# Optimization experiments

Measured on AMD Instinct MI355X. Metric: run time of the kernel, lower is better.

Reference implementation:

```python
import jax, jax.numpy as jnp
from jax import lax
import numpy as np

STEP = 0.01
BS = 32  # blocksize


def conv(x, w, b=None, stride=1, pad=0):
    y = lax.conv_general_dilated(x, w, (stride, stride), [(pad, pad), (pad, pad)],
                                 dimension_numbers=('NCHW', 'OIHW', 'NCHW'))
    if b is not None:
        y = y + b[None, :, None, None]
    return y


def prelu(x, a):
    return jnp.where(x >= 0, x, a * x)


def depth_to_space(x, bs):
    # matches Reshape_Concat_Adap: each [C] pixel vector viewed as (C', bs, bs)
    B, C, h, w = x.shape
    C2 = C // (bs * bs)
    y = x.reshape(B, C2, bs, bs, h, w)
    y = y.transpose(0, 1, 4, 2, 5, 3)  # B, C2, h, bs, w, bs
    return y.reshape(B, C2, h * bs, w * bs)


def setup_inputs() -> dict:
    key = jax.random.key(0)
    ks = jax.random.split(key, 32)

    def W(k, shape):
        fan_in = shape[1] * shape[2] * shape[3]
        return (jax.random.normal(k, shape, jnp.float32) * np.sqrt(2.0 / fan_in)).astype(jnp.float32)

    inp = {
        'x': jax.random.normal(ks[0], (4, 1, 192, 192), jnp.float32),
        'epoch': 1,
        'd1_w': W(ks[1], (16, 1, 4, 4)),
        'd2_w': W(ks[2], (256, 16, 4, 4)),
        'd3_w': W(ks[3], (1024, 256, 2, 2)),
        'd4_w': W(ks[4], (154, 1024, 1, 1)),
        'q1_w': W(ks[5], (154, 154, 1, 1)), 'q1_b': jnp.zeros((154,), jnp.float32),
        'q2_w': W(ks[6], (154, 154, 1, 1)), 'q2_b': jnp.zeros((154,), jnp.float32),
        'q3_w': W(ks[7], (154, 154, 1, 1)), 'q3_b': jnp.zeros((154,), jnp.float32),
        'up_w': W(ks[8], (1024, 154, 1, 1)), 'up_b': jnp.zeros((1024,), jnp.float32),
        'c1_w': W(ks[9], (64, 1, 3, 3)), 'c1_b': jnp.zeros((64,), jnp.float32), 'c1_a': jnp.float32(0.25),
        'c2_w': W(ks[10], (64, 64, 3, 3)), 'c2_b': jnp.zeros((64,), jnp.float32), 'c2_a': jnp.float32(0.25),
        'c3_w': W(ks[11], (64, 64, 3, 3)), 'c3_b': jnp.zeros((64,), jnp.float32), 'c3_a': jnp.float32(0.25),
        'c4_w': W(ks[12], (64, 64, 3, 3)), 'c4_b': jnp.zeros((64,), jnp.float32), 'c4_a': jnp.float32(0.25),
        'c5_w': W(ks[13], (256, 64, 3, 3)), 'c5_b': jnp.zeros((256,), jnp.float32),
    }
    return inp


def reference(x, epoch, d1_w, d2_w, d3_w, d4_w, q1_w, q1_b, q2_w, q2_b, q3_w, q3_b,
              up_w, up_b, c1_w, c1_b, c1_a, c2_w, c2_b, c2_a, c3_w, c3_b, c3_a,
              c4_w, c4_b, c4_a, c5_w, c5_b):
    step = jnp.float32(STEP)
    relu = jax.nn.relu
    # down path
    h = relu(conv(x, d1_w, stride=4))
    h = relu(conv(h, d2_w, stride=4))
    h = relu(conv(h, d3_w, stride=2))
    x4 = conv(h, d4_w)                      # [B,154,H/32,W/32]
    # STE quantize + dequantize
    q = x4 + lax.stop_gradient(jnp.floor(x4 / step) - x4)
    xr = q * step
    t = xr
    t = relu(conv(t, q1_w, q1_b)) + t
    t = relu(conv(t, q2_w, q2_b)) + t
    t = relu(conv(t, q3_w, q3_b)) + t
    x_comp = t + xr
    # upsample to blocksize^2 channels, then depth-to-space
    u = conv(x_comp, up_w, up_b)            # [B,1024,H/32,W/32]
    y = depth_to_space(u, BS)               # [B,1,H,W]
    # refinement CNN
    b1 = prelu(conv(y, c1_w, c1_b, pad=1), c1_a)
    b2 = prelu(conv(b1 + y, c2_w, c2_b, pad=1), c2_a)
    b3 = prelu(conv(b2 + b1, c3_w, c3_b, pad=1), c3_a)
    b4 = prelu(conv(b3 + b2, c4_w, c4_b, pad=1), c4_a)
    b5 = conv(b4 + b3, c5_w, c5_b, pad=1)   # [B,256,H,W]
    B, _, H, Wd = b5.shape
    return (b5.reshape(B, 1, 256, H, Wd), x_comp, x4)
```

## Files before the change

### kernel.cpp

```cpp
#include <hip/hip_runtime.h>
#include <math.h>

#define N_B 4
#define IMG 192
#define P 194

typedef __attribute__((ext_vector_type(8))) short short8;
typedef __attribute__((ext_vector_type(4))) float f32x4;

__device__ __forceinline__ unsigned f2bf(float f) {
  unsigned u = __float_as_uint(f);
  return (u + 0x7fffu + ((u >> 16) & 1u)) >> 16;
}
__device__ __forceinline__ float bf2f(unsigned b) {
  return __uint_as_float(b << 16);
}
__device__ __forceinline__ int swz(int pix) {
  return (pix & 7) << 4;
}
__device__ __forceinline__ void gload_lds16(const void* g, void* l) {
  __builtin_amdgcn_global_load_lds(
      (const __attribute__((address_space(1))) void*)g,
      (__attribute__((address_space(3))) void*)l, 16, 0, 0);
}

__global__ void k_d1(const float* __restrict__ x, const float* __restrict__ w,
                     float* __restrict__ out) {
  int idx = blockIdx.x * 256 + threadIdx.x;
  if (idx >= N_B * 16 * 48 * 48) return;
  int xq = idx % 48; int t = idx / 48; int yq = t % 48; t /= 48;
  int oc = t % 16; int b = t / 16;
  const float* xp = x + (b * IMG + yq * 4) * IMG + xq * 4;
  const float* wp = w + oc * 16;
  float s = 0.f;
#pragma unroll
  for (int dy = 0; dy < 4; ++dy)
#pragma unroll
    for (int dx = 0; dx < 4; ++dx)
      s = fmaf(xp[dy * IMG + dx], wp[dy * 4 + dx], s);
  out[idx] = fmaxf(s, 0.f);
}

__global__ void k_d2(const float* __restrict__ h1, const float* __restrict__ w,
                     float* __restrict__ out) {
  int idx = blockIdx.x * 256 + threadIdx.x;
  if (idx >= N_B * 256 * 12 * 12) return;
  int xq = idx % 12; int t = idx / 12; int yq = t % 12; t /= 12;
  int oc = t % 256; int b = t / 256;
  float s = 0.f;
  for (int ci = 0; ci < 16; ++ci) {
    const float* ip = h1 + ((b * 16 + ci) * 48 + yq * 4) * 48 + xq * 4;
    const float* wp = w + (oc * 16 + ci) * 16;
#pragma unroll
    for (int dy = 0; dy < 4; ++dy)
#pragma unroll
      for (int dx = 0; dx < 4; ++dx)
        s = fmaf(ip[dy * 48 + dx], wp[dy * 4 + dx], s);
  }
  out[((size_t)b * 144 + yq * 12 + xq) * 256 + oc] = fmaxf(s, 0.f);
}

__global__ __launch_bounds__(256) void k_wd3(const float* __restrict__ w,
                                             float* __restrict__ o) {
  int idx = blockIdx.x * 256 + threadIdx.x;
  if (idx >= 4 * 256 * 1024) return;
  int oc = idx & 1023; int ci = (idx >> 10) & 255; int tap = idx >> 18;
  o[idx] = w[((size_t)oc * 256 + ci) * 4 + tap];
}

__global__ __launch_bounds__(256) void k_d3(const float* __restrict__ h2t,
                                            const float* __restrict__ w3p,
                                            float* __restrict__ out) {
  int idx = blockIdx.x * 256 + threadIdx.x;
  if (idx >= N_B * 36 * 1024) return;
  int oc = idx & 1023; int t = idx >> 10; int p6 = t % 36; int b = t / 36;
  int yq = p6 / 6, xq = p6 % 6;
  const float* p00 = h2t + ((size_t)b * 144 + (2 * yq) * 12 + 2 * xq) * 256;
  const float* p01 = p00 + 256;
  const float* p10 = p00 + 12 * 256;
  const float* p11 = p10 + 256;
  const float* w0 = w3p + oc;
  float a0 = 0.f, a1 = 0.f, a2 = 0.f, a3 = 0.f;
  for (int ci = 0; ci < 256; ++ci) {
    a0 = fmaf(p00[ci], w0[(size_t)(0 * 256 + ci) * 1024], a0);
    a1 = fmaf(p01[ci], w0[(size_t)(1 * 256 + ci) * 1024], a1);
    a2 = fmaf(p10[ci], w0[(size_t)(2 * 256 + ci) * 1024], a2);
    a3 = fmaf(p11[ci], w0[(size_t)(3 * 256 + ci) * 1024], a3);
  }
  out[((size_t)b * 36 + p6) * 1024 + oc] = fmaxf((a0 + a1) + (a2 + a3), 0.f);
}

__global__ __launch_bounds__(512) void k_mid(
    const float* __restrict__ h3t, const float* __restrict__ d4_w,
    const float* __restrict__ q1_w, const float* __restrict__ q1_b,
    const float* __restrict__ q2_w, const float* __restrict__ q2_b,
    const float* __restrict__ q3_w, const float* __restrict__ q3_b,
    const float* __restrict__ up_w, const float* __restrict__ up_b,
    float* __restrict__ x4_out, float* __restrict__ xcomp_out,
    float* __restrict__ y_out) {
  __shared__ float hv[1024];
  __shared__ float part[512];
  __shared__ float tv[160];
  __shared__ float xrv[160];
  int blk = blockIdx.x;
  int b = blk / 36, p = blk % 36;
  int tid = threadIdx.x;
  for (int i = tid; i < 1024; i += 512) hv[i] = h3t[(size_t)blk * 1024 + i];
  __syncthreads();
  {
    int half = tid >> 8, oc = tid & 255;
    float s = 0.f;
    if (oc < 154) {
      const float* wp = d4_w + (size_t)oc * 1024 + half * 512;
      const float* hp = hv + half * 512;
      float a0 = 0.f, a1 = 0.f, a2 = 0.f, a3 = 0.f;
      for (int i = 0; i < 512; i += 4) {
        a0 = fmaf(hp[i], wp[i], a0);
        a1 = fmaf(hp[i + 1], wp[i + 1], a1);
        a2 = fmaf(hp[i + 2], wp[i + 2], a2);
        a3 = fmaf(hp[i + 3], wp[i + 3], a3);
      }
      s = (a0 + a1) + (a2 + a3);
    }
    part[tid] = s;
  }
  __syncthreads();
  if (tid < 154) {
    float s = part[tid] + part[tid + 256];
    x4_out[(b * 154 + tid) * 36 + p] = s;
    float q = floorf(s / 0.01f) * 0.01f;
    xrv[tid] = q;
    tv[tid] = q;
  }
  __syncthreads();
  const float* qw[3] = {q1_w, q2_w, q3_w};
  const float* qb[3] = {q1_b, q2_b, q3_b};
  for (int l = 0; l < 3; ++l) {
    float s = 0.f;
    if (tid < 154) {
      const float* wp = qw[l] + (size_t)tid * 154;
      float a0 = 0.f, a1 = 0.f;
      int i = 0;
      for (; i + 1 < 154; i += 2) {
        a0 = fmaf(tv[i], wp[i], a0);
        a1 = fmaf(tv[i + 1], wp[i + 1], a1);
      }
      if (i < 154) a0 = fmaf(tv[i], wp[i], a0);
      s = qb[l][tid] + a0 + a1;
    }
    __syncthreads();
    if (tid < 154) tv[tid] = fmaxf(s, 0.f) + tv[tid];
    __syncthreads();
  }
  if (tid < 154) {
    float xc = tv[tid] + xrv[tid];
    tv[tid] = xc;
    xcomp_out[(b * 154 + tid) * 36 + p] = xc;
  }
  __syncthreads();
  int h = p / 6, w6 = p % 6;
#pragma unroll
  for (int k = 0; k < 2; ++k) {
    int co = k * 512 + tid;
    const float* wp = up_w + (size_t)co * 154;
    float a0 = 0.f, a1 = 0.f;
    int i = 0;
    for (; i + 1 < 154; i += 2) {
      a0 = fmaf(tv[i], wp[i], a0);
      a1 = fmaf(tv[i + 1], wp[i + 1], a1);
    }
    if (i < 154) a0 = fmaf(tv[i], wp[i], a0);
    float s = up_b[co] + a0 + a1;
    int i32 = co >> 5, j = co & 31;
    y_out[(b * IMG + h * 32 + i32) * IMG + w6 * 32 + j] = s;
  }
}

__global__ __launch_bounds__(256) void k_ring(short* s0, short* s1,
                                              short* s2, short* s3) {
  int idx = blockIdx.x * 256 + threadIdx.x;
  if (idx >= 4 * 4 * 772 * 8) return;
  int chunk = idx & 7; int t = idx >> 3;
  int r = t % 772; t /= 772; int b = t % 4; int buf = t / 4;
  int y, x;
  if (r < 194) { y = 0; x = r; }
  else if (r < 388) { y = 193; x = r - 194; }
  else { int q = r - 388; y = 1 + (q >> 1); x = (q & 1) ? 193 : 0; }
  short* p = (buf == 0) ? s0 : (buf == 1) ? s1 : (buf == 2) ? s2 : s3;
  *(uint4*)(p + (((size_t)b * P + y) * P + x) * 64 + chunk * 8) =
      make_uint4(0u, 0u, 0u, 0u);
}

__global__ __launch_bounds__(256) void k_c1b(const float* __restrict__ y,
                                             const float* __restrict__ w,
                                             const float* __restrict__ bias,
                                             const float* __restrict__ a_p,
                                             short* __restrict__ B1,
                                             short* __restrict__ S1) {
  int idx = blockIdx.x * 256 + threadIdx.x;
  if (idx >= N_B * IMG * IMG) return;
  int X = idx % IMG; int t = idx / IMG; int Y = t % IMG; int b = t / IMG;
  float p[9];
#pragma unroll
  for (int dy = 0; dy < 3; ++dy)
#pragma unroll
    for (int dx = 0; dx < 3; ++dx) {
      int gy = Y + dy - 1, gx = X + dx - 1;
      p[dy * 3 + dx] = ((unsigned)gy < (unsigned)IMG && (unsigned)gx < (unsigned)IMG)
                           ? y[(b * IMG + gy) * IMG + gx]
                           : 0.f;
    }
  float a = *a_p;
  float yc = p[4];
  size_t base = (((size_t)b * P + Y + 1) * P + X + 1) * 64;
  for (int oc = 0; oc < 64; oc += 8) {
    unsigned bw[4], sw[4];
#pragma unroll
    for (int j = 0; j < 8; ++j) {
      float s = bias[oc + j];
      const float* wq = w + (oc + j) * 9;
#pragma unroll
      for (int k = 0; k < 9; ++k) s = fmaf(p[k], wq[k], s);
      s = s >= 0.f ? s : a * s;
      float sv = s + yc;
      if (j & 1) { bw[j >> 1] |= f2bf(s) << 16; sw[j >> 1] |= f2bf(sv) << 16; }
      else       { bw[j >> 1] = f2bf(s);        sw[j >> 1] = f2bf(sv); }
    }
    *(uint4*)(B1 + base + oc) = make_uint4(bw[0], bw[1], bw[2], bw[3]);
    *(uint4*)(S1 + base + oc) = make_uint4(sw[0], sw[1], sw[2], sw[3]);
  }
}

__global__ __launch_bounds__(256) void k_wprep4(
    const float* __restrict__ w2, const float* __restrict__ w3,
    const float* __restrict__ w4, const float* __restrict__ w5,
    short* __restrict__ o2, short* __restrict__ o3,
    short* __restrict__ o4, short* __restrict__ o5) {
  int which = blockIdx.y;
  const float* w = (which == 0) ? w2 : (which == 1) ? w3 : (which == 2) ? w4 : w5;
  short* o = (which == 0) ? o2 : (which == 1) ? o3 : (which == 2) ? o4 : o5;
  int OC = (which == 3) ? 256 : 64;
  int idx = blockIdx.x * 256 + threadIdx.x;
  if (idx >= OC * 64 * 9) return;
  int ic = idx & 63; int t = idx >> 6; int r = t % OC; int tap = t / OC;
  int oc = (which < 3) ? (((r >> 2) & 3) * 16 + ((r >> 4) & 3) * 4 + (r & 3)) : r;
  int ks = ic >> 5, lg = (ic >> 3) & 3, j = ic & 7, li = r & 15, ocblk = r >> 4;
  size_t dst = ((size_t)(tap * 2 + ks) * (OC >> 4) + ocblk) * 512 +
               (lg * 16 + li) * 8 + j;
  o[dst] = (short)f2bf(w[((size_t)oc * 64 + ic) * 9 + tap]);
}

template <int MODE>
__global__ __launch_bounds__(256) void k_conv3x3n(
    const short* __restrict__ sin, const short* __restrict__ bprev,
    const short* __restrict__ wbf, const float* __restrict__ bias,
    const float* __restrict__ a_p, short* __restrict__ bout,
    short* __restrict__ sout) {
  __shared__ __align__(16) char smem[300 * 128];
  int tid = threadIdx.x;
  int b = blockIdx.z;
  int x0 = blockIdx.x * 48, y0 = blockIdx.y * 4;
  int w = tid >> 6, lane = tid & 63, li = lane & 15, lg = lane >> 4;

  for (int c = w; c < 38; c += 4) {
    int o = c * 1024 + lane * 16;
    if (o < 300 * 128) {
      int pix = o >> 7;
      int icq = ((o >> 4) & 7) ^ (pix & 7);
      const short* src = sin +
          (((size_t)b * P + y0 + pix / 50) * P + x0 + pix % 50) * 64 + icq * 8;
      gload_lds16(src, smem + c * 1024);
    }
  }
  __syncthreads();

  const short* abase = wbf + (lane << 3);
  const int astride = 64 * 32;

  f32x4 acc[4][3];
#pragma unroll
  for (int mt = 0; mt < 4; ++mt)
#pragma unroll
    for (int nt = 0; nt < 3; ++nt) acc[mt][nt] = (f32x4){0.f, 0.f, 0.f, 0.f};

#define LOADA(s, dst)                                                          \
  {                                                                            \
    const short* p_ = abase + (size_t)(s) * astride;                           \
    _Pragma("unroll") for (int mt = 0; mt < 4; ++mt)                           \
        dst[mt] = *(const short8*)(p_ + mt * 512);                             \
  }
#define LOADB(s, dst)                                                          \
  {                                                                            \
    const int tap_ = (s) >> 1, ks_ = (s) & 1;                                  \
    const int dy_ = tap_ / 3, dx_ = tap_ % 3;                                  \
    _Pragma("unroll") for (int nt = 0; nt < 3; ++nt) {                         \
      int pix_ = (w + dy_) * 50 + nt * 16 + dx_ + li;                          \
      int byte_ = (pix_ * 128 + ks_ * 64 + lg * 16) ^ swz(pix_);               \
      dst[nt] = *(const short8*)(smem + byte_);                                \
    }                                                                          \
  }

  short8 Abuf[2][4];
  short8 Bbuf[3];
  LOADA(0, Abuf[0]);
#pragma unroll
  for (int s = 0; s < 18; ++s) {
    if (s + 1 < 18) LOADA(s + 1, Abuf[(s + 1) & 1]);
    LOADB(s, Bbuf);
    short8* Ac = Abuf[s & 1];
#pragma unroll
    for (int mt = 0; mt < 4; ++mt)
#pragma unroll
      for (int nt = 0; nt < 3; ++nt)
        acc[mt][nt] = __builtin_amdgcn_mfma_f32_16x16x32_bf16(Ac[mt], Bbuf[nt],
                                                              acc[mt][nt], 0, 0, 0);
  }
#undef LOADA
#undef LOADB

  float a = *a_p;
  int gy = y0 + w;
#pragma unroll
  for (int nt = 0; nt < 3; ++nt) {
    int gx = x0 + nt * 16 + li;
    float r[16];
#pragma unroll
    for (int mt = 0; mt < 4; ++mt) {
      float4 bv = *(const float4*)(bias + lg * 16 + mt * 4);
      f32x4 v = acc[mt][nt];
      float t0 = v[0] + bv.x, t1 = v[1] + bv.y, t2 = v[2] + bv.z, t3 = v[3] + bv.w;
      r[mt * 4 + 0] = t0 >= 0.f ? t0 : a * t0;
      r[mt * 4 + 1] = t1 >= 0.f ? t1 : a * t1;
      r[mt * 4 + 2] = t2 >= 0.f ? t2 : a * t2;
      r[mt * 4 + 3] = t3 >= 0.f ? t3 : a * t3;
    }
    size_t pi = (((size_t)b * P + gy + 1) * P + gx + 1) * 64 + lg * 16;
    if (MODE == 0) {
      uint4 u0 = make_uint4(f2bf(r[0]) | (f2bf(r[1]) << 16),
                            f2bf(r[2]) | (f2bf(r[3]) << 16),
                            f2bf(r[4]) | (f2bf(r[5]) << 16),
                            f2bf(r[6]) | (f2bf(r[7]) << 16));
      uint4 u1 = make_uint4(f2bf(r[8]) | (f2bf(r[9]) << 16),
                            f2bf(r[10]) | (f2bf(r[11]) << 16),
                            f2bf(r[12]) | (f2bf(r[13]) << 16),
                            f2bf(r[14]) | (f2bf(r[15]) << 16));
      *(uint4*)(bout + pi) = u0;
      *(uint4*)(bout + pi + 8) = u1;
    }
    uint4 p0 = *(const uint4*)(bprev + pi);
    uint4 p1 = *(const uint4*)(bprev + pi + 8);
    unsigned pw[8] = {p0.x, p0.y, p0.z, p0.w, p1.x, p1.y, p1.z, p1.w};
    unsigned so[8];
#pragma unroll
    for (int k = 0; k < 8; ++k) {
      float s0 = r[2 * k] + bf2f(pw[k] & 0xffffu);
      float s1 = r[2 * k + 1] + bf2f(pw[k] >> 16);
      so[k] = f2bf(s0) | (f2bf(s1) << 16);
    }
    *(uint4*)(sout + pi) = make_uint4(so[0], so[1], so[2], so[3]);
    *(uint4*)(sout + pi + 8) = make_uint4(so[4], so[5], so[6], so[7]);
  }
}

__global__ __launch_bounds__(256) void k_conv3x3b5(
    const short* __restrict__ sin, const short* __restrict__ wbf,
    const float* __restrict__ bias, float* __restrict__ fout) {
  __shared__ __align__(16) char smem[340 * 128];
  int tid = threadIdx.x;
  int g = blockIdx.z & 3, b = blockIdx.z >> 2;
  int x0 = blockIdx.x * 32, y0 = blockIdx.y * 8;
  int w = tid >> 6, lane = tid & 63, li = lane & 15, lg = lane >> 4;

  for (int c = w; c < 43; c += 4) {
    int o = c * 1024 + lane * 16;
    if (o < 340 * 128) {
      int pix = o >> 7;
      int icq = ((o >> 4) & 7) ^ (pix & 7);
      const short* src = sin +
          (((size_t)b * P + y0 + pix / 34) * P + x0 + pix % 34) * 64 + icq * 8;
      gload_lds16(src, smem + c * 1024);
    }
  }
  __syncthreads();

  int row0 = 2 * w;
  const short* abase = wbf + (size_t)(g << 2) * 512 + (lane << 3);
  const int astride = 256 * 32;

  f32x4 acc[4][4];
#pragma unroll
  for (int mt = 0; mt < 4; ++mt)
#pragma unroll
    for (int nt = 0; nt < 4; ++nt) acc[mt][nt] = (f32x4){0.f, 0.f, 0.f, 0.f};

#define LOADA5(s, dst)                                                         \
  {                                                                            \
    const short* p_ = abase + (size_t)(s) * astride;                           \
    _Pragma("unroll") for (int mt = 0; mt < 4; ++mt)                           \
        dst[mt] = *(const short8*)(p_ + mt * 512);                             \
  }
#define LOADB5(s, dst)                                                         \
  {                                                                            \
    const int tap_ = (s) >> 1, ks_ = (s) & 1;                                  \
    const int dy_ = tap_ / 3, dx_ = tap_ % 3;                                  \
    _Pragma("unroll") for (int nt = 0; nt < 4; ++nt) {                         \
      int pix_ = (row0 + (nt >> 1) + dy_) * 34 + (nt & 1) * 16 + dx_ + li;     \
      int byte_ = (pix_ * 128 + ks_ * 64 + lg * 16) ^ swz(pix_);               \
      dst[nt] = *(const short8*)(smem + byte_);                                \
    }                                                                          \
  }

  short8 Abuf[2][4];
  short8 Bbuf[4];
  LOADA5(0, Abuf[0]);
#pragma unroll
  for (int s = 0; s < 18; ++s) {
    if (s + 1 < 18) LOADA5(s + 1, Abuf[(s + 1) & 1]);
    LOADB5(s, Bbuf);
    short8* Ac = Abuf[s & 1];
#pragma unroll
    for (int mt = 0; mt < 4; ++mt)
#pragma unroll
      for (int nt = 0; nt < 4; ++nt)
        acc[mt][nt] = __builtin_amdgcn_mfma_f32_16x16x32_bf16(Bbuf[nt], Ac[mt],
                                                              acc[mt][nt], 0, 0, 0);
  }
#undef LOADA5
#undef LOADB5

#pragma unroll
  for (int nt = 0; nt < 4; ++nt) {
    int gy = y0 + row0 + (nt >> 1);
    int gx = x0 + (nt & 1) * 16 + lg * 4;
#pragma unroll
    for (int mt = 0; mt < 4; ++mt) {
      int oc = g * 64 + mt * 16 + li;
      float bv = bias[oc];
      f32x4 v = acc[mt][nt];
      *(float4*)(fout + (((size_t)b * 256 + oc) * IMG + gy) * IMG + gx) =
          make_float4(v[0] + bv, v[1] + bv, v[2] + bv, v[3] + bv);
    }
  }
}

extern "C" void kernel_launch(void* const* d_in, const int* in_sizes, int n_in,
                              void* d_out, int out_size, void* d_ws, size_t ws_size,
                              hipStream_t stream) {
  const float* x    = (const float*)d_in[0];
  const float* d1_w = (const float*)d_in[2];
  const float* d2_w = (const float*)d_in[3];
  const float* d3_w = (const float*)d_in[4];
  const float* d4_w = (const float*)d_in[5];
  const float* q1_w = (const float*)d_in[6];
  const float* q1_b = (const float*)d_in[7];
  const float* q2_w = (const float*)d_in[8];
  const float* q2_b = (const float*)d_in[9];
  const float* q3_w = (const float*)d_in[10];
  const float* q3_b = (const float*)d_in[11];
  const float* up_w = (const float*)d_in[12];
  const float* up_b = (const float*)d_in[13];
  const float* c1_w = (const float*)d_in[14];
  const float* c1_b = (const float*)d_in[15];
  const float* c1_a = (const float*)d_in[16];
  const float* c2_w = (const float*)d_in[17];
  const float* c2_b = (const float*)d_in[18];
  const float* c2_a = (const float*)d_in[19];
  const float* c3_w = (const float*)d_in[20];
  const float* c3_b = (const float*)d_in[21];
  const float* c3_a = (const float*)d_in[22];
  const float* c4_w = (const float*)d_in[23];
  const float* c4_b = (const float*)d_in[24];
  const float* c4_a = (const float*)d_in[25];
  const float* c5_w = (const float*)d_in[26];
  const float* c5_b = (const float*)d_in[27];

  float* out = (float*)d_out;
  float* ws  = (float*)d_ws;

  const size_t B5  = (size_t)N_B * 256 * IMG * IMG;
  const size_t SML = (size_t)N_B * 154 * 36;
  float* out_b5    = out;
  float* out_xcomp = out + B5;
  float* out_x4    = out + B5 + SML;

  const size_t PADBUF = (size_t)N_B * P * P * 64 / 2;
  size_t off = 0;
  float* h1   = ws + off; off += (size_t)N_B * 16 * 48 * 48;
  float* h2t  = ws + off; off += (size_t)N_B * 144 * 256;
  float* h3t  = ws + off; off += (size_t)N_B * 36 * 1024;
  float* w3p  = ws + off; off += (size_t)4 * 256 * 1024;
  float* ybuf = ws + off; off += (size_t)N_B * IMG * IMG;
  short* sl0  = (short*)(ws + off); off += PADBUF;
  short* sl1  = (short*)(ws + off); off += PADBUF;
  short* sl2  = (short*)(ws + off); off += PADBUF;
  short* sl3  = (short*)(ws + off); off += PADBUF;
  short* wb2  = (short*)(ws + off); off += 9 * 64 * 64 / 2;
  short* wb3  = (short*)(ws + off); off += 9 * 64 * 64 / 2;
  short* wb4  = (short*)(ws + off); off += 9 * 64 * 64 / 2;
  short* wb5  = (short*)(ws + off); off += 9 * 256 * 64 / 2;

  dim3 wg((9 * 256 * 64 + 255) / 256, 4);
  k_wprep4<<<wg, 256, 0, stream>>>(c2_w, c3_w, c4_w, c5_w, wb2, wb3, wb4, wb5);
  k_wd3<<<(4 * 256 * 1024 + 255) / 256, 256, 0, stream>>>(d3_w, w3p);
  k_ring<<<(4 * 4 * 772 * 8 + 255) / 256, 256, 0, stream>>>(sl0, sl1, sl2, sl3);

  k_d1<<<(N_B * 16 * 48 * 48 + 255) / 256, 256, 0, stream>>>(x, d1_w, h1);
  k_d2<<<(N_B * 256 * 12 * 12 + 255) / 256, 256, 0, stream>>>(h1, d2_w, h2t);
  k_d3<<<(N_B * 36 * 1024 + 255) / 256, 256, 0, stream>>>(h2t, w3p, h3t);

  k_mid<<<N_B * 36, 512, 0, stream>>>(h3t, d4_w, q1_w, q1_b, q2_w, q2_b,
                                      q3_w, q3_b, up_w, up_b,
                                      out_x4, out_xcomp, ybuf);

  k_c1b<<<(N_B * IMG * IMG + 255) / 256, 256, 0, stream>>>(ybuf, c1_w, c1_b, c1_a,
                                                           sl1 , sl0 );

  dim3 cg(4, 48, N_B);
  k_conv3x3n<0><<<cg, 256, 0, stream>>>(sl0, sl1, wb2, c2_b, c2_a, sl2, sl3);
  k_conv3x3n<0><<<cg, 256, 0, stream>>>(sl3, sl2, wb3, c3_b, c3_a, sl1, sl0);
  k_conv3x3n<1><<<cg, 256, 0, stream>>>(sl0, sl1, wb4, c4_b, c4_a, nullptr, sl3);
  dim3 cg5(IMG / 32, IMG / 8, N_B * 4);
  k_conv3x3b5<<<cg5, 256, 0, stream>>>(sl3, wb5, c5_b, out_b5);
}
```

Measured before the change: 316.2 us.

## Merge prep kernels into one launch and retile final conv to 48x4 tiles

Folds the three setup kernels (weight bf16 repack, d3 weight transpose, padding ring zeroing) into a single launch to cut launch overhead. It also retiles the final 64->256 conv from 32x8 pixel tiles to 48x4 tiles, matching the other 3x3 convs. Each wave now handles one row of three 16-pixel groups instead of two rows of two. This shrinks the shared-memory halo and the accumulators, which may help occupancy. The cost is fewer MFMAs per A-fragment load and more blocks to schedule.

```diff
diff --git a/kernel.cpp b/kernel.cpp
--- a/kernel.cpp
+++ b/kernel.cpp
@@ -58,14 +58,6 @@
         s = fmaf(ip[dy * 48 + dx], wp[dy * 4 + dx], s);
   }
   out[((size_t)b * 144 + yq * 12 + xq) * 256 + oc] = fmaxf(s, 0.f);
-}
-
-__global__ __launch_bounds__(256) void k_wd3(const float* __restrict__ w,
-                                             float* __restrict__ o) {
-  int idx = blockIdx.x * 256 + threadIdx.x;
-  if (idx >= 4 * 256 * 1024) return;
-  int oc = idx & 1023; int ci = (idx >> 10) & 255; int tap = idx >> 18;
-  o[idx] = w[((size_t)oc * 256 + ci) * 4 + tap];
 }
 
 __global__ __launch_bounds__(256) void k_d3(const float* __restrict__ h2t,
@@ -176,21 +168,6 @@
   }
 }
 
-__global__ __launch_bounds__(256) void k_ring(short* s0, short* s1,
-                                              short* s2, short* s3) {
-  int idx = blockIdx.x * 256 + threadIdx.x;
-  if (idx >= 4 * 4 * 772 * 8) return;
-  int chunk = idx & 7; int t = idx >> 3;
-  int r = t % 772; t /= 772; int b = t % 4; int buf = t / 4;
-  int y, x;
-  if (r < 194) { y = 0; x = r; }
-  else if (r < 388) { y = 193; x = r - 194; }
-  else { int q = r - 388; y = 1 + (q >> 1); x = (q & 1) ? 193 : 0; }
-  short* p = (buf == 0) ? s0 : (buf == 1) ? s1 : (buf == 2) ? s2 : s3;
-  *(uint4*)(p + (((size_t)b * P + y) * P + x) * 64 + chunk * 8) =
-      make_uint4(0u, 0u, 0u, 0u);
-}
-
 __global__ __launch_bounds__(256) void k_c1b(const float* __restrict__ y,
                                              const float* __restrict__ w,
                                              const float* __restrict__ bias,
@@ -231,23 +208,56 @@
   }
 }
 
-__global__ __launch_bounds__(256) void k_wprep4(
+#define WPA (64 * 64 * 9)
+#define WPB (256 * 64 * 9)
+#define WD3N (4 * 256 * 1024)
+#define RINGN (4 * 4 * 772 * 8)
+#define PREPN (3 * WPA + WPB + WD3N + RINGN)
+__global__ __launch_bounds__(256) void k_prep(
     const float* __restrict__ w2, const float* __restrict__ w3,
     const float* __restrict__ w4, const float* __restrict__ w5,
+    const float* __restrict__ d3w,
     short* __restrict__ o2, short* __restrict__ o3,
-    short* __restrict__ o4, short* __restrict__ o5) {
-  int which = blockIdx.y;
-  const float* w = (which == 0) ? w2 : (which == 1) ? w3 : (which == 2) ? w4 : w5;
-  short* o = (which == 0) ? o2 : (which == 1) ? o3 : (which == 2) ? o4 : o5;
-  int OC = (which == 3) ? 256 : 64;
+    short* __restrict__ o4, short* __restrict__ o5,
+    float* __restrict__ w3p,
+    short* __restrict__ s0, short* __restrict__ s1,
+    short* __restrict__ s2, short* __restrict__ s3) {
   int idx = blockIdx.x * 256 + threadIdx.x;
-  if (idx >= OC * 64 * 9) return;
-  int ic = idx & 63; int t = idx >> 6; int r = t % OC; int tap = t / OC;
-  int oc = (which < 3) ? (((r >> 2) & 3) * 16 + ((r >> 4) & 3) * 4 + (r & 3)) : r;
-  int ks = ic >> 5, lg = (ic >> 3) & 3, j = ic & 7, li = r & 15, ocblk = r >> 4;
-  size_t dst = ((size_t)(tap * 2 + ks) * (OC >> 4) + ocblk) * 512 +
-               (lg * 16 + li) * 8 + j;
-  o[dst] = (short)f2bf(w[((size_t)oc * 64 + ic) * 9 + tap]);
+  if (idx < 3 * WPA + WPB) {
+    int which, id;
+    if (idx < WPA) { which = 0; id = idx; }
+    else if (idx < 2 * WPA) { which = 1; id = idx - WPA; }
+    else if (idx < 3 * WPA) { which = 2; id = idx - 2 * WPA; }
+    else { which = 3; id = idx - 3 * WPA; }
+    const float* w = (which == 0) ? w2 : (which == 1) ? w3 : (which == 2) ? w4 : w5;
+    short* o = (which == 0) ? o2 : (which == 1) ? o3 : (which == 2) ? o4 : o5;
+    int OC = (which == 3) ? 256 : 64;
+    int ic = id & 63; int t = id >> 6; int r = t % OC; int tap = t / OC;
+    int oc = (which < 3) ? (((r >> 2) & 3) * 16 + ((r >> 4) & 3) * 4 + (r & 3)) : r;
+    int ks = ic >> 5, lg = (ic >> 3) & 3, j = ic & 7, li = r & 15, ocblk = r >> 4;
+    size_t dst = ((size_t)(tap * 2 + ks) * (OC >> 4) + ocblk) * 512 +
+                 (lg * 16 + li) * 8 + j;
+    o[dst] = (short)f2bf(w[((size_t)oc * 64 + ic) * 9 + tap]);
+    return;
+  }
+  idx -= 3 * WPA + WPB;
+  if (idx < WD3N) {
+    int oc = idx & 1023; int ci = (idx >> 10) & 255; int tap = idx >> 18;
+    w3p[idx] = d3w[((size_t)oc * 256 + ci) * 4 + tap];
+    return;
+  }
+  idx -= WD3N;
+  if (idx < RINGN) {
+    int chunk = idx & 7; int t = idx >> 3;
+    int r = t % 772; t /= 772; int b = t % 4; int buf = t / 4;
+    int y, x;
+    if (r < 194) { y = 0; x = r; }
+    else if (r < 388) { y = 193; x = r - 194; }
+    else { int q = r - 388; y = 1 + (q >> 1); x = (q & 1) ? 193 : 0; }
+    short* p = (buf == 0) ? s0 : (buf == 1) ? s1 : (buf == 2) ? s2 : s3;
+    *(uint4*)(p + (((size_t)b * P + y) * P + x) * 64 + chunk * 8) =
+        make_uint4(0u, 0u, 0u, 0u);
+  }
 }
 
 template <int MODE>
@@ -362,36 +372,35 @@
   }
 }
 
-__global__ __launch_bounds__(256) void k_conv3x3b5(
+__global__ __launch_bounds__(256) void k_conv5n(
     const short* __restrict__ sin, const short* __restrict__ wbf,
     const float* __restrict__ bias, float* __restrict__ fout) {
-  __shared__ __align__(16) char smem[340 * 128];
+  __shared__ __align__(16) char smem[300 * 128];
   int tid = threadIdx.x;
   int g = blockIdx.z & 3, b = blockIdx.z >> 2;
-  int x0 = blockIdx.x * 32, y0 = blockIdx.y * 8;
+  int x0 = blockIdx.x * 48, y0 = blockIdx.y * 4;
   int w = tid >> 6, lane = tid & 63, li = lane & 15, lg = lane >> 4;
 
-  for (int c = w; c < 43; c += 4) {
+  for (int c = w; c < 38; c += 4) {
     int o = c * 1024 + lane * 16;
-    if (o < 340 * 128) {
+    if (o < 300 * 128) {
       int pix = o >> 7;
       int icq = ((o >> 4) & 7) ^ (pix & 7);
       const short* src = sin +
-          (((size_t)b * P + y0 + pix / 34) * P + x0 + pix % 34) * 64 + icq * 8;
+          (((size_t)b * P + y0 + pix / 50) * P + x0 + pix % 50) * 64 + icq * 8;
       gload_lds16(src, smem + c * 1024);
     }
   }
   __syncthreads();
 
-  int row0 = 2 * w;
   const short* abase = wbf + (size_t)(g << 2) * 512 + (lane << 3);
   const int astride = 256 * 32;
 
-  f32x4 acc[4][4];
+  f32x4 acc[4][3];
 #pragma unroll
   for (int mt = 0; mt < 4; ++mt)
 #pragma unroll
-    for (int nt = 0; nt < 4; ++nt) acc[mt][nt] = (f32x4){0.f, 0.f, 0.f, 0.f};
+    for (int nt = 0; nt < 3; ++nt) acc[mt][nt] = (f32x4){0.f, 0.f, 0.f, 0.f};
 
 #define LOADA5(s, dst)                                                         \
   {                                                                            \
@@ -403,15 +412,15 @@
   {                                                                            \
     const int tap_ = (s) >> 1, ks_ = (s) & 1;                                  \
     const int dy_ = tap_ / 3, dx_ = tap_ % 3;                                  \
-    _Pragma("unroll") for (int nt = 0; nt < 4; ++nt) {                         \
-      int pix_ = (row0 + (nt >> 1) + dy_) * 34 + (nt & 1) * 16 + dx_ + li;     \
+    _Pragma("unroll") for (int nt = 0; nt < 3; ++nt) {                         \
+      int pix_ = (w + dy_) * 50 + nt * 16 + dx_ + li;                          \
       int byte_ = (pix_ * 128 + ks_ * 64 + lg * 16) ^ swz(pix_);               \
       dst[nt] = *(const short8*)(smem + byte_);                                \
     }                                                                          \
   }
 
   short8 Abuf[2][4];
-  short8 Bbuf[4];
+  short8 Bbuf[3];
   LOADA5(0, Abuf[0]);
 #pragma unroll
   for (int s = 0; s < 18; ++s) {
@@ -421,17 +430,17 @@
 #pragma unroll
     for (int mt = 0; mt < 4; ++mt)
 #pragma unroll
-      for (int nt = 0; nt < 4; ++nt)
+      for (int nt = 0; nt < 3; ++nt)
         acc[mt][nt] = __builtin_amdgcn_mfma_f32_16x16x32_bf16(Bbuf[nt], Ac[mt],
                                                               acc[mt][nt], 0, 0, 0);
   }
 #undef LOADA5
 #undef LOADB5
 
-#pragma unroll
-  for (int nt = 0; nt < 4; ++nt) {
-    int gy = y0 + row0 + (nt >> 1);
-    int gx = x0 + (nt & 1) * 16 + lg * 4;
+  int gy = y0 + w;
+#pragma unroll
+  for (int nt = 0; nt < 3; ++nt) {
+    int gx = x0 + nt * 16 + lg * 4;
 #pragma unroll
     for (int mt = 0; mt < 4; ++mt) {
       int oc = g * 64 + mt * 16 + li;
@@ -499,10 +508,9 @@
   short* wb4  = (short*)(ws + off); off += 9 * 64 * 64 / 2;
   short* wb5  = (short*)(ws + off); off += 9 * 256 * 64 / 2;
 
-  dim3 wg((9 * 256 * 64 + 255) / 256, 4);
-  k_wprep4<<<wg, 256, 0, stream>>>(c2_w, c3_w, c4_w, c5_w, wb2, wb3, wb4, wb5);
-  k_wd3<<<(4 * 256 * 1024 + 255) / 256, 256, 0, stream>>>(d3_w, w3p);
-  k_ring<<<(4 * 4 * 772 * 8 + 255) / 256, 256, 0, stream>>>(sl0, sl1, sl2, sl3);
+  k_prep<<<(PREPN + 255) / 256, 256, 0, stream>>>(
+      c2_w, c3_w, c4_w, c5_w, d3_w, wb2, wb3, wb4, wb5, w3p,
+      sl0, sl1, sl2, sl3);
 
   k_d1<<<(N_B * 16 * 48 * 48 + 255) / 256, 256, 0, stream>>>(x, d1_w, h1);
   k_d2<<<(N_B * 256 * 12 * 12 + 255) / 256, 256, 0, stream>>>(h1, d2_w, h2t);
@@ -519,6 +527,6 @@
   k_conv3x3n<0><<<cg, 256, 0, stream>>>(sl0, sl1, wb2, c2_b, c2_a, sl2, sl3);
   k_conv3x3n<0><<<cg, 256, 0, stream>>>(sl3, sl2, wb3, c3_b, c3_a, sl1, sl0);
   k_conv3x3n<1><<<cg, 256, 0, stream>>>(sl0, sl1, wb4, c4_b, c4_a, nullptr, sl3);
-  dim3 cg5(IMG / 32, IMG / 8, N_B * 4);
-  k_conv3x3b5<<<cg5, 256, 0, stream>>>(sl3, wb5, c5_b, out_b5);
-}
+  dim3 cg5(4, 48, N_B * 4);
+  k_conv5n<<<cg5, 256, 0, stream>>>(sl3, wb5, c5_b, out_b5);
+}
```

Result: faster. 309.1 us (-2.2%).
